# Optimization experiments

Hardware: AMD Instinct MI355X
Metric: run time of the kernel (lower is better)

Reference implementation:

```python
import jax, jax.numpy as jnp
import numpy as np

STOCH, DETER, HID, OBS, ACT = 32, 512, 512, 18, 4
MIN_STD, EPS, UPD_BIAS = 0.1, 1e-3, -1.0


def _ln(x, g, b):
    m = x.mean(-1, keepdims=True)
    v = ((x - m) ** 2).mean(-1, keepdims=True)
    return (x - m) * jax.lax.rsqrt(v + EPS) * g + b


def setup_inputs() -> dict:
    key = jax.random.key(0)
    ks = jax.random.split(key, 10)
    B, T = 256, 256
    def w(k, i, o):
        return jax.random.normal(k, (i, o), jnp.float32) / np.float32(np.sqrt(i))
    return {
        "obs": jax.random.normal(ks[0], (B, T, OBS), jnp.float32),
        "action": jax.random.normal(ks[1], (B, T, ACT), jnp.float32),
        "is_first": jax.random.randint(ks[2], (B, T), 0, 2, jnp.int32),
        "w_prior_in": w(ks[3], STOCH + ACT, HID),
        "g_prior_in": jnp.ones(HID, jnp.float32),
        "bb_prior_in": jnp.zeros(HID, jnp.float32),
        "w_gru": w(ks[4], HID + DETER, 3 * DETER),
        "g_gru": jnp.ones(3 * DETER, jnp.float32),
        "bb_gru": jnp.zeros(3 * DETER, jnp.float32),
        "w_prior_out": w(ks[5], DETER, HID),
        "g_prior_out": jnp.ones(HID, jnp.float32),
        "bb_prior_out": jnp.zeros(HID, jnp.float32),
        "w_prior_stats": w(ks[6], HID, 2 * STOCH),
        "b_prior_stats": jnp.zeros(2 * STOCH, jnp.float32),
        "w_post": w(ks[7], DETER + OBS, HID),
        "g_post": jnp.ones(HID, jnp.float32),
        "bb_post": jnp.zeros(HID, jnp.float32),
        "w_post_stats": w(ks[8], HID, 2 * STOCH),
        "b_post_stats": jnp.zeros(2 * STOCH, jnp.float32),
        "initial_deter": 0.1 * jax.random.normal(ks[9], (1, DETER), jnp.float32),
    }


def reference(obs, action, is_first,
              w_prior_in, g_prior_in, bb_prior_in,
              w_gru, g_gru, bb_gru,
              w_prior_out, g_prior_out, bb_prior_out,
              w_prior_stats, b_prior_stats,
              w_post, g_post, bb_post,
              w_post_stats, b_post_stats,
              initial_deter):
    """RSSM.observe with sample=False. Returns (B, T, 2*(DETER+3*STOCH)):
    concat of post[deter,stoch,mean,std] and prior[deter,stoch,mean,std];
    stoch == mean since dist.mean is used."""
    B = obs.shape[0]
    # learned initial state (identical for every batch row / reset)
    deter0 = jnp.tanh(initial_deter)                                  # (1, DETER)
    h0 = jax.nn.silu(_ln(deter0 @ w_prior_out, g_prior_out, bb_prior_out))
    s0 = h0 @ w_prior_stats + b_prior_stats
    init_mean, _ = jnp.split(s0, 2, axis=-1)                          # (1, STOCH)

    def step(carry, xs):
        deter, stoch = carry
        o_t, a_t, f_t = xs
        mask = (f_t > 0)[:, None]
        deter = jnp.where(mask, deter0, deter)
        stoch = jnp.where(mask, init_mean, stoch)
        a_t = jnp.where(mask, 0.0, a_t)
        # prior_in
        h = jax.nn.silu(_ln(jnp.concatenate([stoch, a_t], -1) @ w_prior_in,
                            g_prior_in, bb_prior_in))
        # GRU cell (depth=1)
        gates = _ln(jnp.concatenate([h, deter], -1) @ w_gru, g_gru, bb_gru)
        r, c, u = jnp.split(gates, 3, axis=-1)
        r = jax.nn.sigmoid(r)
        u = jax.nn.sigmoid(u + UPD_BIAS)
        cand = jax.nn.silu(r * c)
        deter = u * cand + (1.0 - u) * deter
        # prior stats
        h2 = jax.nn.silu(_ln(deter @ w_prior_out, g_prior_out, bb_prior_out))
        ps = h2 @ w_prior_stats + b_prior_stats
        pm, psd = jnp.split(ps, 2, axis=-1)
        psd = jax.nn.softplus(psd) + MIN_STD
        # posterior
        h3 = jax.nn.silu(_ln(jnp.concatenate([deter, o_t], -1) @ w_post,
                             g_post, bb_post))
        qs = h3 @ w_post_stats + b_post_stats
        qm, qsd = jnp.split(qs, 2, axis=-1)
        qsd = jax.nn.softplus(qsd) + MIN_STD
        out = jnp.concatenate([deter, qm, qm, qsd, deter, pm, pm, psd], -1)
        return (deter, qm), out

    carry0 = (jnp.broadcast_to(deter0, (B, DETER)),
              jnp.broadcast_to(init_mean, (B, STOCH)))
    xs = (obs.swapaxes(0, 1), action.swapaxes(0, 1), is_first.swapaxes(0, 1))
    _, ys = jax.lax.scan(step, carry0, xs)   # (T, B, 2*(DETER+3*STOCH))
    return ys.swapaxes(0, 1)
```

## Files before the change

### kernel.cpp

```cpp
#include <hip/hip_runtime.h>
#include <hip/hip_cooperative_groups.h>

namespace cg = cooperative_groups;

#define TT 256
#define GRID 256
#define BDIM 256

typedef unsigned short u16;
typedef unsigned int u32;
typedef __attribute__((ext_vector_type(8))) short bf16x8;
typedef __attribute__((ext_vector_type(4))) float f32x4;

struct P {
  const float* obs; const float* action; const int* is_first;
  const float* w_prior_in; const float* g_prior_in; const float* bb_prior_in;
  const float* w_gru; const float* g_gru; const float* bb_gru;
  const float* w_prior_out; const float* g_prior_out; const float* bb_prior_out;
  const float* w_prior_stats; const float* b_prior_stats;
  const float* w_post; const float* g_post; const float* bb_post;
  const float* w_post_stats; const float* b_post_stats;
  const float* initial_deter;
  float* out;
  u16 *WgT3;
  u16 *W2T3;
  u16 *WsT3;
  float *deter0, *init_mean;
  int *segb, *segt0, *nact;
  float *deter;
  float *stoch;
  u16 *xg;
  float *gates;
  u16 *dox;
  float *hraw;
  u16 *h2;
  int CH;
};

__device__ __forceinline__ float b2f(u16 u) {
  union { float f; u32 i; } v; v.i = ((u32)u) << 16; return v.f;
}
__device__ __forceinline__ u16 f2b(float f) {
  union { float f; u32 i; } v; v.f = f;
  u32 r = v.i + 0x7FFF + ((v.i >> 16) & 1);
  return (u16)(r >> 16);
}
__device__ __forceinline__ float sigm(float x) { return 1.f / (1.f + __expf(-x)); }
__device__ __forceinline__ float splus(float x) { return x > 15.f ? x : log1pf(__expf(x)); }

__device__ __forceinline__ void h_from_x(const P& p, int i, float xv, int lane) {
  float a0[8];
  #pragma unroll
  for (int c = 0; c < 8; ++c) a0[c] = 0.f;
  #pragma unroll 4
  for (int j = 0; j < 36; ++j) {
    float s = __shfl(xv, j, 64);
    const float* wr = p.w_prior_in + j * 512 + lane;
    #pragma unroll
    for (int c = 0; c < 8; ++c) a0[c] = fmaf(s, wr[c << 6], a0[c]);
  }
  float sm = 0.f, sq = 0.f;
  #pragma unroll
  for (int c = 0; c < 8; ++c) { sm += a0[c]; sq += a0[c] * a0[c]; }
  #pragma unroll
  for (int o = 32; o; o >>= 1) { sm += __shfl_xor(sm, o); sq += __shfl_xor(sq, o); }
  float m = sm * (1.f / 512.f);
  float rs = rsqrtf(sq * (1.f / 512.f) - m * m + 1e-3f);
  size_t rowb = (size_t)i * 3072;
  #pragma unroll
  for (int c = 0; c < 8; ++c) {
    int col = lane + (c << 6);
    float v = (a0[c] - m) * rs * p.g_prior_in[col] + p.bb_prior_in[col];
    v = v * sigm(v);
    u16 hi = f2b(v); u16 lo = f2b(v - b2f(hi));
    p.xg[rowb + col] = hi;
    p.xg[rowb + 1024 + col] = lo;
    p.xg[rowb + 2048 + col] = hi;
  }
}

__global__ void k_weights(P p) {
  const int E1 = 1536 * 1024, E2 = 1024 * 544, E3 = 128 * 1024;
  const int total = E1 + E2 + E3;
  for (int idx = blockIdx.x * blockDim.x + threadIdx.x; idx < total;
       idx += gridDim.x * blockDim.x) {
    float w; u16* dst; int kk, kappa;
    if (idx < E1) {
      int n = idx >> 10; kk = idx & 1023; kappa = 1024;
      w = p.w_gru[kk * 1536 + n];
      dst = p.WgT3 + (size_t)n * 3072;
    } else if (idx < E1 + E2) {
      int t = idx - E1; int n = t / 544; kk = t - n * 544; kappa = 544;
      if (n < 512) w = (kk < 512) ? p.w_prior_out[kk * 512 + n] : 0.f;
      else         w = (kk < 530) ? p.w_post[kk * 512 + (n - 512)] : 0.f;
      dst = p.W2T3 + (size_t)n * 1632;
    } else {
      int t = idx - E1 - E2; int n = t >> 10; kk = t & 1023; kappa = 1024;
      if (n < 64) w = (kk < 512) ? p.w_prior_stats[kk * 64 + n] : 0.f;
      else        w = (kk >= 512) ? p.w_post_stats[(kk - 512) * 64 + (n - 64)] : 0.f;
      dst = p.WsT3 + (size_t)n * 3072;
    }
    u16 hi = f2b(w); u16 lo = f2b(w - b2f(hi));
    dst[kk] = hi; dst[kappa + kk] = hi; dst[2 * kappa + kk] = lo;
  }
}

__global__ void k_init_state(P p) {
  __shared__ float d0s[512], tmp[512], red[256];
  int tid = threadIdx.x;
  for (int n = tid; n < 512; n += 256) { d0s[n] = tanhf(p.initial_deter[n]); p.deter0[n] = d0s[n]; }
  __syncthreads();
  for (int n = tid; n < 512; n += 256) {
    float s = 0.f;
    for (int d = 0; d < 512; ++d) s = fmaf(d0s[d], p.w_prior_out[d * 512 + n], s);
    tmp[n] = s;
  }
  __syncthreads();
  float ls = 0.f, lq = 0.f;
  for (int n = tid; n < 512; n += 256) { ls += tmp[n]; lq += tmp[n] * tmp[n]; }
  red[tid] = ls; __syncthreads();
  for (int s = 128; s; s >>= 1) { if (tid < s) red[tid] += red[tid + s]; __syncthreads(); }
  float m = red[0] * (1.f / 512.f); __syncthreads();
  red[tid] = lq; __syncthreads();
  for (int s = 128; s; s >>= 1) { if (tid < s) red[tid] += red[tid + s]; __syncthreads(); }
  float rs = rsqrtf(red[0] * (1.f / 512.f) - m * m + 1e-3f); __syncthreads();
  for (int n = tid; n < 512; n += 256) {
    float h = (tmp[n] - m) * rs * p.g_prior_out[n] + p.bb_prior_out[n];
    tmp[n] = h * sigm(h);
  }
  __syncthreads();
  if (tid < 32) {
    float s = 0.f;
    for (int d = 0; d < 512; ++d) s = fmaf(tmp[d], p.w_prior_stats[d * 64 + tid], s);
    p.init_mean[tid] = s + p.b_prior_stats[tid];
  }
}

__global__ void k_segments(P p) {
  __shared__ int hist[257], off[258], cur[257];
  int tid = threadIdx.x;
  for (int i = tid; i < 257; i += 256) hist[i] = 0;
  __syncthreads();
  int b = tid;
  { int t = 0;
    while (t < TT) {
      int t0 = t; t++;
      while (t < TT && p.is_first[b * TT + t] == 0) t++;
      atomicAdd(&hist[t - t0], 1);
    } }
  __syncthreads();
  if (tid == 0) {
    int run = 0;
    for (int len = 256; len >= 0; --len) { off[len] = run; run += hist[len]; }
  }
  __syncthreads();
  for (int i = tid; i < 257; i += 256) { cur[i] = off[i]; p.nact[i] = off[i]; }
  __syncthreads();
  { int t = 0;
    while (t < TT) {
      int t0 = t; t++;
      while (t < TT && p.is_first[b * TT + t] == 0) t++;
      int idx = atomicAdd(&cur[t - t0], 1);
      p.segb[idx] = b; p.segt0[idx] = t0;
    } }
}

__device__ void gemm_tiles(const u16* A, int lda, const u16* B, int ldb,
                           float* C, int ldc, int M, int ntn, int K3,
                           u16* Ab, u16* Bb, int bid, int nb, int tid) {
  const int wave = tid >> 6, lane = tid & 63, quad = lane >> 4, l15 = lane & 15;
  const int wr = (wave & 1) << 6, wc = (wave >> 1) << 6;
  const int ntm = (M + 127) >> 7;
  const int njobs = ntm * ntn;
  for (int j = bid; j < njobs; j += nb) {
    int tm = j / ntn, tn = j - tm * ntn;
    int r0 = tm << 7, c0 = tn << 7;
    f32x4 acc[4][4];
    #pragma unroll
    for (int a = 0; a < 4; ++a)
      #pragma unroll
      for (int bq = 0; bq < 4; ++bq) acc[a][bq] = f32x4{0.f, 0.f, 0.f, 0.f};
    for (int k0 = 0; k0 < K3; k0 += 32) {
      __syncthreads();
      #pragma unroll
      for (int s = 0; s < 2; ++s) {
        int ch = tid + (s << 8);
        int row = ch >> 2, ko = (ch & 3) << 3;
        *(uint4*)&Ab[(row << 5) + ko] =
            *(const uint4*)(A + (size_t)(r0 + row) * lda + k0 + ko);
        *(uint4*)&Bb[(row << 5) + ko] =
            *(const uint4*)(B + (size_t)(c0 + row) * ldb + k0 + ko);
      }
      __syncthreads();
      bf16x8 af[4], bf[4];
      #pragma unroll
      for (int s2 = 0; s2 < 4; ++s2) {
        af[s2] = *(const bf16x8*)&Ab[((wr + (s2 << 4) + l15) << 5) + (quad << 3)];
        bf[s2] = *(const bf16x8*)&Bb[((wc + (s2 << 4) + l15) << 5) + (quad << 3)];
      }
      #pragma unroll
      for (int mi = 0; mi < 4; ++mi)
        #pragma unroll
        for (int ni = 0; ni < 4; ++ni)
          acc[mi][ni] = __builtin_amdgcn_mfma_f32_16x16x32_bf16(af[mi], bf[ni], acc[mi][ni], 0, 0, 0);
    }
    #pragma unroll
    for (int mi = 0; mi < 4; ++mi)
      #pragma unroll
      for (int ni = 0; ni < 4; ++ni)
        #pragma unroll
        for (int r = 0; r < 4; ++r)
          C[(size_t)(r0 + wr + (mi << 4) + (quad << 2) + r) * ldc
            + c0 + wc + (ni << 4) + l15] = acc[mi][ni][r];
  }
}

__global__ void __launch_bounds__(BDIM, 2) k_main(P p) {
  cg::grid_group grid = cg::this_grid();
  __shared__ u16 Ab[128 * 32], Bb[128 * 32];
  const int tid = threadIdx.x;
  const int bid = blockIdx.x, nb = gridDim.x;
  const int wave = tid >> 6, lane = tid & 63, quad = lane >> 4, l15 = lane & 15;
  const int gw = (bid << 2) + wave, nwv = nb << 2;
  const int CH = p.CH;
  const int S_total = p.nact[0];

  for (int base = 0; base < S_total; base += CH) {
    for (int k = 0;; ++k) {
      int Sk = p.nact[k] - base; Sk = Sk > CH ? CH : Sk;
      if (Sk <= 0) break;

      for (int i = gw; i < Sk; i += nwv) {
        int gi = base + i;
        int b = p.segb[gi], t0 = p.segt0[gi];
        float xv = 0.f;
        if (k == 0) {
          size_t rowb = (size_t)i * 3072;
          #pragma unroll
          for (int c = 0; c < 8; ++c) {
            int d = lane + (c << 6);
            float v = p.deter0[d];
            p.deter[(size_t)i * 512 + d] = v;
            u16 hi = f2b(v); u16 lo = f2b(v - b2f(hi));
            p.xg[rowb + 512 + d] = hi;
            p.xg[rowb + 1536 + d] = lo;
            p.xg[rowb + 2560 + d] = hi;
          }
          int ff = p.is_first[b * TT + t0];
          if (lane < 32) xv = p.init_mean[lane];
          else if (lane < 36) xv = (ff > 0) ? 0.f : p.action[((size_t)b * TT + t0) * 4 + (lane - 32)];
        } else {
          if (lane < 32) xv = p.stoch[(size_t)i * 32 + lane];
          else if (lane < 36) xv = p.action[((size_t)b * TT + t0 + k) * 4 + (lane - 32)];
        }
        h_from_x(p, i, xv, lane);
      }
      grid.sync();

      gemm_tiles(p.xg, 3072, p.WgT3, 3072, p.gates, 1536, Sk, 12, 3072,
                 Ab, Bb, bid, nb, tid);
      grid.sync();

      for (int i = gw; i < Sk; i += nwv) {
        const float* grow = p.gates + (size_t)i * 1536;
        float g[24];
        float sm = 0.f, sq = 0.f;
        #pragma unroll
        for (int c = 0; c < 24; ++c) {
          g[c] = grow[lane + (c << 6)];
          sm += g[c]; sq += g[c] * g[c];
        }
        #pragma unroll
        for (int o = 32; o; o >>= 1) { sm += __shfl_xor(sm, o); sq += __shfl_xor(sq, o); }
        float m = sm * (1.f / 1536.f);
        float rs = rsqrtf(sq * (1.f / 1536.f) - m * m + 1e-3f);
        int gi = base + i;
        int b = p.segb[gi], t = p.segt0[gi] + k;
        float* orow = p.out + ((size_t)b * TT + t) * 1216;
        size_t rowx = (size_t)i * 3072, rowd = (size_t)i * 1632;
        #pragma unroll
        for (int c = 0; c < 8; ++c) {
          int d = lane + (c << 6);
          float gr = (g[c]      - m) * rs * p.g_gru[d]        + p.bb_gru[d];
          float gc = (g[c + 8]  - m) * rs * p.g_gru[512 + d]  + p.bb_gru[512 + d];
          float gu = (g[c + 16] - m) * rs * p.g_gru[1024 + d] + p.bb_gru[1024 + d];
          float r_ = sigm(gr);
          float u_ = sigm(gu - 1.0f);
          float rc = r_ * gc;
          float cand = rc * sigm(rc);
          float dp = p.deter[(size_t)i * 512 + d];
          float dn = u_ * cand + (1.f - u_) * dp;
          p.deter[(size_t)i * 512 + d] = dn;
          orow[d] = dn; orow[608 + d] = dn;
          u16 hi = f2b(dn); u16 lo = f2b(dn - b2f(hi));
          p.xg[rowx + 512 + d] = hi;
          p.xg[rowx + 1536 + d] = lo;
          p.xg[rowx + 2560 + d] = hi;
          p.dox[rowd + d] = hi;
          p.dox[rowd + 544 + d] = lo;
          p.dox[rowd + 1088 + d] = hi;
        }
        if (lane < 32) {
          float ov = (lane < 18) ? p.obs[((size_t)b * TT + t) * 18 + lane] : 0.f;
          u16 hi = f2b(ov); u16 lo = f2b(ov - b2f(hi));
          p.dox[rowd + 512 + lane] = hi;
          p.dox[rowd + 1056 + lane] = lo;
          p.dox[rowd + 1600 + lane] = hi;
        }
      }
      grid.sync();

      gemm_tiles(p.dox, 1632, p.W2T3, 1632, p.hraw, 1024, Sk, 8, 1632,
                 Ab, Bb, bid, nb, tid);
      grid.sync();

      for (int i = gw; i < Sk; i += nwv) {
        size_t rowh = (size_t)i * 3072;
        #pragma unroll
        for (int hh = 0; hh < 2; ++hh) {
          const float* hb = p.hraw + (size_t)i * 1024 + (hh << 9);
          const float* gv = hh ? p.g_post : p.g_prior_out;
          const float* bv = hh ? p.bb_post : p.bb_prior_out;
          float v[8];
          float sm = 0.f, sq = 0.f;
          #pragma unroll
          for (int c = 0; c < 8; ++c) {
            v[c] = hb[lane + (c << 6)];
            sm += v[c]; sq += v[c] * v[c];
          }
          #pragma unroll
          for (int o = 32; o; o >>= 1) { sm += __shfl_xor(sm, o); sq += __shfl_xor(sq, o); }
          float m = sm * (1.f / 512.f);
          float rs = rsqrtf(sq * (1.f / 512.f) - m * m + 1e-3f);
          #pragma unroll
          for (int c = 0; c < 8; ++c) {
            int d = lane + (c << 6);
            float x = (v[c] - m) * rs * gv[d] + bv[d];
            x = x * sigm(x);
            int col = (hh << 9) + d;
            u16 hi = f2b(x); u16 lo = f2b(x - b2f(hi));
            p.h2[rowh + col] = hi;
            p.h2[rowh + 1024 + col] = lo;
            p.h2[rowh + 2048 + col] = hi;
          }
        }
      }
      grid.sync();

      {
        const int sr = (wave & 1) << 4, sc = (wave >> 1) << 6;
        int njobs = (Sk + 31) >> 5;
        for (int j = bid; j < njobs; j += nb) {
          int r0 = j << 5;
          f32x4 acc[4];
          #pragma unroll
          for (int z = 0; z < 4; ++z) acc[z] = f32x4{0.f, 0.f, 0.f, 0.f};
          for (int k0 = 0; k0 < 3072; k0 += 32) {
            __syncthreads();
            if (tid < 128) {
              int row = tid >> 2, ko = (tid & 3) << 3;
              *(uint4*)&Ab[(row << 5) + ko] =
                  *(const uint4*)(p.h2 + (size_t)(r0 + row) * 3072 + k0 + ko);
            }
            #pragma unroll
            for (int s = 0; s < 2; ++s) {
              int ch = tid + (s << 8);
              int row = ch >> 2, ko = (ch & 3) << 3;
              *(uint4*)&Bb[(row << 5) + ko] =
                  *(const uint4*)(p.WsT3 + (size_t)row * 3072 + k0 + ko);
            }
            __syncthreads();
            bf16x8 af = *(const bf16x8*)&Ab[((sr + l15) << 5) + (quad << 3)];
            #pragma unroll
            for (int ns = 0; ns < 4; ++ns) {
              bf16x8 bf = *(const bf16x8*)&Bb[((sc + (ns << 4) + l15) << 5) + (quad << 3)];
              acc[ns] = __builtin_amdgcn_mfma_f32_16x16x32_bf16(af, bf, acc[ns], 0, 0, 0);
            }
          }
          #pragma unroll
          for (int ns = 0; ns < 4; ++ns)
            #pragma unroll
            for (int r = 0; r < 4; ++r) {
              int i = r0 + sr + (quad << 2) + r;
              int col = sc + (ns << 4) + l15;
              if (i < Sk) {
                float v = acc[ns][r];
                int gi = base + i;
                int b = p.segb[gi], t = p.segt0[gi] + k;
                float* orow = p.out + ((size_t)b * TT + t) * 1216;
                if (col < 32) {
                  v += p.b_prior_stats[col];
                  orow[1120 + col] = v; orow[1152 + col] = v;
                } else if (col < 64) {
                  v = splus(v + p.b_prior_stats[col]) + 0.1f;
                  orow[1184 + col - 32] = v;
                } else if (col < 96) {
                  v += p.b_post_stats[col - 64];
                  orow[512 + col - 64] = v; orow[544 + col - 64] = v;
                  p.stoch[(size_t)i * 32 + (col - 64)] = v;
                } else {
                  v = splus(v + p.b_post_stats[col - 64]) + 0.1f;
                  orow[576 + col - 96] = v;
                }
              }
            }
        }
      }
      grid.sync();
    }
  }
}

extern "C" void kernel_launch(void* const* d_in, const int* in_sizes, int n_in,
                              void* d_out, int out_size, void* d_ws, size_t ws_size,
                              hipStream_t stream) {
  P p;
  p.obs = (const float*)d_in[0];
  p.action = (const float*)d_in[1];
  p.is_first = (const int*)d_in[2];
  p.w_prior_in = (const float*)d_in[3];
  p.g_prior_in = (const float*)d_in[4];
  p.bb_prior_in = (const float*)d_in[5];
  p.w_gru = (const float*)d_in[6];
  p.g_gru = (const float*)d_in[7];
  p.bb_gru = (const float*)d_in[8];
  p.w_prior_out = (const float*)d_in[9];
  p.g_prior_out = (const float*)d_in[10];
  p.bb_prior_out = (const float*)d_in[11];
  p.w_prior_stats = (const float*)d_in[12];
  p.b_prior_stats = (const float*)d_in[13];
  p.w_post = (const float*)d_in[14];
  p.g_post = (const float*)d_in[15];
  p.bb_post = (const float*)d_in[16];
  p.w_post_stats = (const float*)d_in[17];
  p.b_post_stats = (const float*)d_in[18];
  p.initial_deter = (const float*)d_in[19];
  p.out = (float*)d_out;

  char* w = (char*)d_ws;
  auto alloc = [&](size_t bytes) -> char* {
    char* r = w; w += (bytes + 255) & ~(size_t)255; return r;
  };
  p.WgT3 = (u16*)alloc((size_t)1536 * 3072 * 2);
  p.W2T3 = (u16*)alloc((size_t)1024 * 1632 * 2);
  p.WsT3 = (u16*)alloc((size_t)128 * 3072 * 2);
  p.deter0    = (float*)alloc(512 * 4);
  p.init_mean = (float*)alloc(32 * 4);
  p.segb  = (int*)alloc((size_t)65536 * 4);
  p.segt0 = (int*)alloc((size_t)65536 * 4);
  p.nact  = (int*)alloc(257 * 4);
  size_t used = (size_t)(w - (char*)d_ws);
  size_t avail = ws_size > used ? ws_size - used : 0;
  long long ch = (long long)(avail / 28672);
  if (ch > 8192) ch = 8192;
  ch &= ~127LL;
  if (ch < 128) ch = 128;
  p.CH = (int)ch;
  p.deter = (float*)alloc((size_t)p.CH * 512 * 4);
  p.stoch = (float*)alloc((size_t)p.CH * 32 * 4);
  p.xg    = (u16*)alloc((size_t)p.CH * 3072 * 2);
  p.gates = (float*)alloc((size_t)p.CH * 1536 * 4);
  p.dox   = (u16*)alloc((size_t)p.CH * 1632 * 2);
  p.hraw  = (float*)alloc((size_t)p.CH * 1024 * 4);
  p.h2    = (u16*)alloc((size_t)p.CH * 3072 * 2);

  k_weights<<<dim3(256), dim3(256), 0, stream>>>(p);
  k_init_state<<<dim3(1), dim3(256), 0, stream>>>(p);
  k_segments<<<dim3(1), dim3(256), 0, stream>>>(p);
  void* args[] = { &p };
  hipLaunchCooperativeKernel(reinterpret_cast<void*>(&k_main), dim3(GRID), dim3(BDIM),
                             args, 0, stream);
}
```

Before: 10.91 ms.

## Double-buffer GEMM tiles with async global-to-LDS loads

Replaces the register-staged global-to-shared copies in the gate/hidden GEMMs and the stats GEMM with `global_load_lds` direct-to-LDS loads into two alternating buffers. The next K-slice is prefetched while MFMAs consume the current one, which leaves one barrier per iteration instead of two. The aim is to hide global-load latency behind matrix math and save register traffic. It doubles LDS use per block and depends on the barrier waiting for the outstanding LDS-DMA writes.

```diff
diff --git a/kernel.cpp b/kernel.cpp
--- a/kernel.cpp
+++ b/kernel.cpp
@@ -11,6 +11,10 @@
 typedef unsigned int u32;
 typedef __attribute__((ext_vector_type(8))) short bf16x8;
 typedef __attribute__((ext_vector_type(4))) float f32x4;
+
+#define GLL(g, l) __builtin_amdgcn_global_load_lds( \
+    (const __attribute__((address_space(1))) void*)(g), \
+    (__attribute__((address_space(3))) void*)(l), 16, 0, 0)
 
 struct P {
   const float* obs; const float* action; const int* is_first;
@@ -167,31 +171,41 @@
 
 __device__ void gemm_tiles(const u16* A, int lda, const u16* B, int ldb,
                            float* C, int ldc, int M, int ntn, int K3,
-                           u16* Ab, u16* Bb, int bid, int nb, int tid) {
+                           u16* lds, int bid, int nb, int tid) {
   const int wave = tid >> 6, lane = tid & 63, quad = lane >> 4, l15 = lane & 15;
   const int wr = (wave & 1) << 6, wc = (wave >> 1) << 6;
   const int ntm = (M + 127) >> 7;
   const int njobs = ntm * ntn;
+  const int row0 = tid >> 2, ko0 = (tid & 3) << 3;
+  u16* const la0 = lds + (wave << 9);
+  u16* const la1 = lds + 2048 + (wave << 9);
+  u16* const lb0 = lds + 8192 + (wave << 9);
+  u16* const lb1 = lds + 8192 + 2048 + (wave << 9);
   for (int j = bid; j < njobs; j += nb) {
     int tm = j / ntn, tn = j - tm * ntn;
     int r0 = tm << 7, c0 = tn << 7;
+    const u16* ga0 = A + (size_t)(r0 + row0) * lda + ko0;
+    const u16* ga1 = A + (size_t)(r0 + row0 + 64) * lda + ko0;
+    const u16* gb0 = B + (size_t)(c0 + row0) * ldb + ko0;
+    const u16* gb1 = B + (size_t)(c0 + row0 + 64) * ldb + ko0;
     f32x4 acc[4][4];
     #pragma unroll
     for (int a = 0; a < 4; ++a)
       #pragma unroll
       for (int bq = 0; bq < 4; ++bq) acc[a][bq] = f32x4{0.f, 0.f, 0.f, 0.f};
+    __syncthreads();
+    GLL(ga0, la0); GLL(ga1, la1); GLL(gb0, lb0); GLL(gb1, lb1);
+    int buf = 0;
     for (int k0 = 0; k0 < K3; k0 += 32) {
       __syncthreads();
-      #pragma unroll
-      for (int s = 0; s < 2; ++s) {
-        int ch = tid + (s << 8);
-        int row = ch >> 2, ko = (ch & 3) << 3;
-        *(uint4*)&Ab[(row << 5) + ko] =
-            *(const uint4*)(A + (size_t)(r0 + row) * lda + k0 + ko);
-        *(uint4*)&Bb[(row << 5) + ko] =
-            *(const uint4*)(B + (size_t)(c0 + row) * ldb + k0 + ko);
-      }
-      __syncthreads();
+      if (k0 + 32 < K3) {
+        int bo = (buf ^ 1) << 12;
+        int o = k0 + 32;
+        GLL(ga0 + o, la0 + bo); GLL(ga1 + o, la1 + bo);
+        GLL(gb0 + o, lb0 + bo); GLL(gb1 + o, lb1 + bo);
+      }
+      const u16* Ab = lds + (buf << 12);
+      const u16* Bb = lds + 8192 + (buf << 12);
       bf16x8 af[4], bf[4];
       #pragma unroll
       for (int s2 = 0; s2 < 4; ++s2) {
@@ -203,6 +217,7 @@
         #pragma unroll
         for (int ni = 0; ni < 4; ++ni)
           acc[mi][ni] = __builtin_amdgcn_mfma_f32_16x16x32_bf16(af[mi], bf[ni], acc[mi][ni], 0, 0, 0);
+      buf ^= 1;
     }
     #pragma unroll
     for (int mi = 0; mi < 4; ++mi)
@@ -217,7 +232,7 @@
 
 __global__ void __launch_bounds__(BDIM, 2) k_main(P p) {
   cg::grid_group grid = cg::this_grid();
-  __shared__ u16 Ab[128 * 32], Bb[128 * 32];
+  __shared__ u16 lds[16384];
   const int tid = threadIdx.x;
   const int bid = blockIdx.x, nb = gridDim.x;
   const int wave = tid >> 6, lane = tid & 63, quad = lane >> 4, l15 = lane & 15;
@@ -258,7 +273,7 @@
       grid.sync();
 
       gemm_tiles(p.xg, 3072, p.WgT3, 3072, p.gates, 1536, Sk, 12, 3072,
-                 Ab, Bb, bid, nb, tid);
+                 lds, bid, nb, tid);
       grid.sync();
 
       for (int i = gw; i < Sk; i += nwv) {
@@ -311,7 +326,7 @@
       grid.sync();
 
       gemm_tiles(p.dox, 1632, p.W2T3, 1632, p.hraw, 1024, Sk, 8, 1632,
-                 Ab, Bb, bid, nb, tid);
+                 lds, bid, nb, tid);
       grid.sync();
 
       for (int i = gw; i < Sk; i += nwv) {
@@ -349,33 +364,41 @@
 
       {
         const int sr = (wave & 1) << 4, sc = (wave >> 1) << 6;
+        const int frow = tid >> 2, fko = (tid & 3) << 3;
         int njobs = (Sk + 31) >> 5;
+        const u16* gbF0 = p.WsT3 + (size_t)frow * 3072 + fko;
+        const u16* gbF1 = p.WsT3 + (size_t)(frow + 64) * 3072 + fko;
+        u16* const lFA = lds + (wave << 9);
+        u16* const lFB0 = lds + 2048 + (wave << 9);
+        u16* const lFB1 = lds + 2048 + 2048 + (wave << 9);
         for (int j = bid; j < njobs; j += nb) {
           int r0 = j << 5;
+          const u16* gaF = p.h2 + (size_t)(r0 + frow) * 3072 + fko;
           f32x4 acc[4];
           #pragma unroll
           for (int z = 0; z < 4; ++z) acc[z] = f32x4{0.f, 0.f, 0.f, 0.f};
+          __syncthreads();
+          if (tid < 128) GLL(gaF, lFA);
+          GLL(gbF0, lFB0); GLL(gbF1, lFB1);
+          int buf = 0;
           for (int k0 = 0; k0 < 3072; k0 += 32) {
             __syncthreads();
-            if (tid < 128) {
-              int row = tid >> 2, ko = (tid & 3) << 3;
-              *(uint4*)&Ab[(row << 5) + ko] =
-                  *(const uint4*)(p.h2 + (size_t)(r0 + row) * 3072 + k0 + ko);
+            if (k0 + 32 < 3072) {
+              int nbuf = buf ^ 1;
+              int o = k0 + 32;
+              if (tid < 128) GLL(gaF + o, lFA + (nbuf << 10));
+              GLL(gbF0 + o, lFB0 + (nbuf << 12));
+              GLL(gbF1 + o, lFB1 + (nbuf << 12));
             }
-            #pragma unroll
-            for (int s = 0; s < 2; ++s) {
-              int ch = tid + (s << 8);
-              int row = ch >> 2, ko = (ch & 3) << 3;
-              *(uint4*)&Bb[(row << 5) + ko] =
-                  *(const uint4*)(p.WsT3 + (size_t)row * 3072 + k0 + ko);
-            }
-            __syncthreads();
-            bf16x8 af = *(const bf16x8*)&Ab[((sr + l15) << 5) + (quad << 3)];
+            const u16* FA = lds + (buf << 10);
+            const u16* FB = lds + 2048 + (buf << 12);
+            bf16x8 af = *(const bf16x8*)&FA[((sr + l15) << 5) + (quad << 3)];
             #pragma unroll
             for (int ns = 0; ns < 4; ++ns) {
-              bf16x8 bf = *(const bf16x8*)&Bb[((sc + (ns << 4) + l15) << 5) + (quad << 3)];
+              bf16x8 bf = *(const bf16x8*)&FB[((sc + (ns << 4) + l15) << 5) + (quad << 3)];
               acc[ns] = __builtin_amdgcn_mfma_f32_16x16x32_bf16(af, bf, acc[ns], 0, 0, 0);
             }
+            buf ^= 1;
           }
           #pragma unroll
           for (int ns = 0; ns < 4; ++ns)
```

Result: faster. 10.58 ms (-3.0%).
